# Optimization experiments

Measured on AMD Instinct MI355X. Metric: run time of the kernel, lower is better.

The kernel has to match this reference:

```python
import jax, jax.numpy as jnp
import numpy as np

N_NEURONS = 100000
N_EDGES = 5000000
N_TYPES = 64
N_DM = 512
BATCH = 16
LAYER_NUMBER = 4  # number of connectome hops


def setup_inputs() -> dict:
    key = jax.random.key(0)
    ks = jax.random.split(key, 11)
    return {
        "x": jax.random.normal(ks[0], (N_NEURONS, BATCH), dtype=jnp.float32),
        "type_weight": jax.random.normal(ks[1], (N_TYPES,), dtype=jnp.float32),
        "type_bias": jax.random.normal(ks[2], (N_TYPES,), dtype=jnp.float32),
        # shared_weights = log1p(synapse counts) -> positive; use uniform
        "edge_weights": jax.random.uniform(ks[3], (N_EDGES,), dtype=jnp.float32),
        "dm_vals": jax.random.uniform(ks[4], (N_DM,), dtype=jnp.float32),
        "fc_w": jax.random.normal(ks[5], (1, N_DM), dtype=jnp.float32) * 0.04,
        "fc_b": jax.random.normal(ks[6], (1,), dtype=jnp.float32),
        "cell_type_indices": jax.random.randint(ks[7], (N_NEURONS,), 0, N_TYPES),
        "edge_rows": jax.random.randint(ks[8], (N_EDGES,), 0, N_NEURONS),
        "edge_cols": jax.random.randint(ks[9], (N_EDGES,), 0, N_NEURONS),
        "dm_cols": jax.random.randint(ks[10], (N_DM,), 0, N_NEURONS),
    }


def reference(x, type_weight, type_bias, edge_weights, dm_vals, fc_w, fc_b,
              cell_type_indices, edge_rows, edge_cols, dm_cols):
    # RetinaConnectionLayer: per-cell-type 1->1 linear (gathered scale + bias)
    h = x * type_weight[cell_type_indices][:, None] + type_bias[cell_type_indices][:, None]
    # AdultConnectome / SparseMatrixMul: repeated sparse COO matmul h = A @ h
    # with shared per-edge weights, applied layer_number times.
    for _ in range(LAYER_NUMBER):
        contrib = edge_weights[:, None] * h[edge_cols]          # [E, B] gather
        h = jax.ops.segment_sum(contrib, edge_rows, num_segments=N_NEURONS)
    # torch.sparse.mm(decision_making_tensor, h): row-selection sparse matrix
    y = dm_vals[:, None] * h[dm_cols]                           # [N_DM, B]
    # final_fc over the decision-neuron axis
    out = y.T @ fc_w.T + fc_b                                   # [B, 1]
    return out
```

## Files before the change

### kernel.cpp

```cpp
#include <hip/hip_runtime.h>

#define NN 100000
#define NE 5000000
#define NB 16
#define NDM 512

#define RPB 1024
#define NBUCKET 98
#define CAP 55296
#define CHUNK 8192
#define NCHUNK ((NE + CHUNK - 1) / CHUNK)
#define SUB 16
#define NWAVE 16

__global__ void setup(const float* __restrict__ dmv, const int* __restrict__ dmc,
                      const float* __restrict__ fcw,
                      float* __restrict__ u0, int* __restrict__ cursor) {
    int t = threadIdx.x;
    if (t < NDM) atomicAdd(&u0[dmc[t]], dmv[t] * fcw[t]);
    if (t < NBUCKET) cursor[t] = t * CAP;
}

__global__ void scatter_fused(const int* __restrict__ er, const int* __restrict__ ec,
                              const float* __restrict__ ew,
                              const float* __restrict__ u0, float* __restrict__ u1,
                              int* __restrict__ cursor, int2* __restrict__ packed) {
    __shared__ int hist[NWAVE][NBUCKET];
    __shared__ __align__(16) int sdst[CHUNK];
    __shared__ int lbase[NBUCKET];
    __shared__ int lrank[NBUCKET];
    int tid = threadIdx.x;
    int wv = tid >> 6;
    for (int k = tid; k < NWAVE * NBUCKET; k += 1024) hist[k / NBUCKET][k % NBUCKET] = 0;
    __syncthreads();
    int base = blockIdx.x * CHUNK;
    int n = min(CHUNK, NE - base);
    const int4* ec4 = (const int4*)(ec + base);
    for (int k = tid; k < (n >> 2); k += 1024) {
        int4 c = ec4[k];
        ((int4*)sdst)[k] = c;
        atomicAdd(&hist[wv][c.x >> 10], 1);
        atomicAdd(&hist[wv][c.y >> 10], 1);
        atomicAdd(&hist[wv][c.z >> 10], 1);
        atomicAdd(&hist[wv][c.w >> 10], 1);
    }
    __syncthreads();
    for (int b = tid; b < NBUCKET; b += 1024) {
        int c = 0;
        #pragma unroll
        for (int w = 0; w < NWAVE; ++w) c += hist[w][b];
        lbase[b] = c ? atomicAdd(&cursor[b], c) : 0;
        lrank[b] = 0;
    }
    __syncthreads();
    const int4*   er4 = (const int4*)(er + base);
    const float4* ew4 = (const float4*)(ew + base);
    for (int k = tid; k < (n >> 2); k += 1024) {
        int4 r = er4[k];
        float4 w = ew4[k];
        int k4 = 4 * k;
        int d, bk, rk;
        float a;
        d = sdst[k4];     bk = d >> 10; rk = atomicAdd(&lrank[bk], 1);
        packed[lbase[bk] + rk] = make_int2(((d & 1023) << 17) | r.x, __float_as_int(w.x));
        a = u0[r.x]; if (a != 0.f) atomicAdd(&u1[d], w.x * a);
        d = sdst[k4 + 1]; bk = d >> 10; rk = atomicAdd(&lrank[bk], 1);
        packed[lbase[bk] + rk] = make_int2(((d & 1023) << 17) | r.y, __float_as_int(w.y));
        a = u0[r.y]; if (a != 0.f) atomicAdd(&u1[d], w.y * a);
        d = sdst[k4 + 2]; bk = d >> 10; rk = atomicAdd(&lrank[bk], 1);
        packed[lbase[bk] + rk] = make_int2(((d & 1023) << 17) | r.z, __float_as_int(w.z));
        a = u0[r.z]; if (a != 0.f) atomicAdd(&u1[d], w.z * a);
        d = sdst[k4 + 3]; bk = d >> 10; rk = atomicAdd(&lrank[bk], 1);
        packed[lbase[bk] + rk] = make_int2(((d & 1023) << 17) | r.w, __float_as_int(w.w));
        a = u0[r.w]; if (a != 0.f) atomicAdd(&u1[d], w.w * a);
    }
}

__global__ void spmv_sorted(const int* __restrict__ cursor,
                            const int2* __restrict__ packed,
                            const float* __restrict__ wc, float* __restrict__ wn) {
    __shared__ float acc[RPB];
    int bucket = blockIdx.x >> 4;
    int sub = blockIdx.x & (SUB - 1);
    int t = threadIdx.x;
    #pragma unroll
    for (int k = 0; k < 4; ++k) acc[t + 256 * k] = 0.f;
    __syncthreads();
    int s = bucket * CAP;
    int e = cursor[bucket];
    int cnt = e - s;
    int slice = (cnt + SUB - 1) >> 4;
    int mys = s + sub * slice;
    int mye = min(mys + slice, e);
    int i = mys + t;
    for (; i + 768 < mye; i += 1024) {
        int2 p0 = packed[i];
        int2 p1 = packed[i + 256];
        int2 p2 = packed[i + 512];
        int2 p3 = packed[i + 768];
        float v0 = __int_as_float(p0.y) * wc[p0.x & 0x1FFFF];
        float v1 = __int_as_float(p1.y) * wc[p1.x & 0x1FFFF];
        float v2 = __int_as_float(p2.y) * wc[p2.x & 0x1FFFF];
        float v3 = __int_as_float(p3.y) * wc[p3.x & 0x1FFFF];
        if (v0 != 0.f) atomicAdd(&acc[p0.x >> 17], v0);
        if (v1 != 0.f) atomicAdd(&acc[p1.x >> 17], v1);
        if (v2 != 0.f) atomicAdd(&acc[p2.x >> 17], v2);
        if (v3 != 0.f) atomicAdd(&acc[p3.x >> 17], v3);
    }
    for (; i < mye; i += 256) {
        int2 p = packed[i];
        float v = __int_as_float(p.y) * wc[p.x & 0x1FFFF];
        if (v != 0.f) atomicAdd(&acc[p.x >> 17], v);
    }
    __syncthreads();
    #pragma unroll
    for (int k = 0; k < 4; ++k) {
        int row = bucket * RPB + t + 256 * k;
        float a = acc[t + 256 * k];
        if (a != 0.f && row < NN) atomicAdd(&wn[row], a);
    }
}

__global__ void final_dot(const float* __restrict__ x, const float* __restrict__ tw,
                          const float* __restrict__ tb, const int* __restrict__ ct,
                          const float* __restrict__ u,
                          float* __restrict__ acc_out) {
    __shared__ float s[512];
    __shared__ float sred[256][4];
    __shared__ float sbias[4];
    int tid = threadIdx.x;
    int base = blockIdx.x * 512;
    int nrows = min(512, NN - base);
    float accb = 0.f;
    for (int r = tid; r < nrows; r += 256) {
        int n = base + r;
        float un = u[n];
        int t = ct[n];
        s[r] = un * tw[t];
        accb = fmaf(un, tb[t], accb);
    }
    __syncthreads();
    float a0 = 0.f, a1 = 0.f, a2 = 0.f, a3 = 0.f;
    int j = (tid & 3) * 4;
    for (int r = tid >> 2; r < nrows; r += 64) {
        float4 xv = *(const float4*)&x[(size_t)(base + r) * NB + j];
        float sv = s[r];
        a0 = fmaf(sv, xv.x, a0);
        a1 = fmaf(sv, xv.y, a1);
        a2 = fmaf(sv, xv.z, a2);
        a3 = fmaf(sv, xv.w, a3);
    }
    sred[tid][0] = a0; sred[tid][1] = a1; sred[tid][2] = a2; sred[tid][3] = a3;
    for (int off = 32; off; off >>= 1) accb += __shfl_down(accb, off);
    if ((tid & 63) == 0) sbias[tid >> 6] = accb;
    __syncthreads();
    if (tid < 16) {
        int q = tid >> 2, k = tid & 3;
        float sum = 0.f;
        for (int i = 0; i < 64; ++i) sum += sred[q + 4 * i][k];
        atomicAdd(&acc_out[tid], sum);
    }
    if (tid == 16)
        atomicAdd(&acc_out[16], sbias[0] + sbias[1] + sbias[2] + sbias[3]);
}

__global__ void finalize(const float* __restrict__ acc, const float* __restrict__ fcb,
                         float* __restrict__ out) {
    int b = threadIdx.x;
    if (b < NB) out[b] = acc[b] + acc[16] + fcb[0];
}

extern "C" void kernel_launch(void* const* d_in, const int* in_sizes, int n_in,
                              void* d_out, int out_size, void* d_ws, size_t ws_size,
                              hipStream_t stream) {
    const float* x   = (const float*)d_in[0];
    const float* tw  = (const float*)d_in[1];
    const float* tb  = (const float*)d_in[2];
    const float* ew  = (const float*)d_in[3];
    const float* dmv = (const float*)d_in[4];
    const float* fcw = (const float*)d_in[5];
    const float* fcb = (const float*)d_in[6];
    const int* ct  = (const int*)d_in[7];
    const int* er  = (const int*)d_in[8];
    const int* ec  = (const int*)d_in[9];
    const int* dmc = (const int*)d_in[10];
    float* out = (float*)d_out;

    char* ws = (char*)d_ws;
    float* u   = (float*)ws;
    float* acc = u + 5 * (size_t)NN;
    size_t zero_bytes = (5 * (size_t)NN + 32) * 4;
    ws += zero_bytes;
    int* cursor = (int*)ws;         ws += 128 * 4;
    ws = (char*)(((uintptr_t)ws + 15) & ~(uintptr_t)15);
    int2* packed = (int2*)ws;

    hipMemsetAsync(u, 0, zero_bytes, stream);

    setup<<<1, 512, 0, stream>>>(dmv, dmc, fcw, u, cursor);

    scatter_fused<<<NCHUNK, 1024, 0, stream>>>(er, ec, ew, u, u + NN, cursor, packed);

    for (int l = 1; l < 4; ++l) {
        spmv_sorted<<<NBUCKET * SUB, 256, 0, stream>>>(cursor, packed,
                                                       u + (size_t)l * NN,
                                                       u + (size_t)(l + 1) * NN);
    }

    final_dot<<<(NN + 511) / 512, 256, 0, stream>>>(x, tw, tb, ct, u + 4 * (size_t)NN, acc);
    finalize<<<1, 64, 0, stream>>>(acc, fcb, out);
}
```

Measured before the change: 170.5 us.

## Stage bucket-sorted edges in shared memory before coalesced global write-out

The scatter kernel now does the edge and weight loads in a single pass, holding the edges in registers, and takes each edge's local rank from the histogram atomic. A shared-memory prefix sum then places every entry into a block-local sorted buffer, which is copied to the global packed array in bucket-contiguous runs. This replaces the global scatter that used a per-edge LDS rank atomic and issued random 8-byte stores. In exchange the kernel uses more shared memory (about 64KB plus extra), needs more registers, and adds several barriers for the scan.

```diff
diff --git a/kernel.cpp b/kernel.cpp
--- a/kernel.cpp
+++ b/kernel.cpp
@@ -21,58 +21,100 @@
     if (t < NBUCKET) cursor[t] = t * CAP;
 }
 
-__global__ void scatter_fused(const int* __restrict__ er, const int* __restrict__ ec,
-                              const float* __restrict__ ew,
-                              const float* __restrict__ u0, float* __restrict__ u1,
-                              int* __restrict__ cursor, int2* __restrict__ packed) {
+__global__ void __launch_bounds__(1024, 8)
+scatter_fused(const int* __restrict__ er, const int* __restrict__ ec,
+              const float* __restrict__ ew,
+              const float* __restrict__ u0, float* __restrict__ u1,
+              int* __restrict__ cursor, int2* __restrict__ packed) {
     __shared__ int hist[NWAVE][NBUCKET];
-    __shared__ __align__(16) int sdst[CHUNK];
-    __shared__ int lbase[NBUCKET];
-    __shared__ int lrank[NBUCKET];
+    __shared__ int2 pval[CHUNK];
+    __shared__ unsigned char sbk[CHUNK];
+    __shared__ int lbloc[128];
+    __shared__ int gbase[NBUCKET];
+    __shared__ int ctot[NBUCKET];
     int tid = threadIdx.x;
     int wv = tid >> 6;
     for (int k = tid; k < NWAVE * NBUCKET; k += 1024) hist[k / NBUCKET][k % NBUCKET] = 0;
     __syncthreads();
     int base = blockIdx.x * CHUNK;
     int n = min(CHUNK, NE - base);
-    const int4* ec4 = (const int4*)(ec + base);
-    for (int k = tid; k < (n >> 2); k += 1024) {
-        int4 c = ec4[k];
-        ((int4*)sdst)[k] = c;
-        atomicAdd(&hist[wv][c.x >> 10], 1);
-        atomicAdd(&hist[wv][c.y >> 10], 1);
-        atomicAdd(&hist[wv][c.z >> 10], 1);
-        atomicAdd(&hist[wv][c.w >> 10], 1);
-    }
-    __syncthreads();
-    for (int b = tid; b < NBUCKET; b += 1024) {
+    int nq = n >> 2;
+    const int4*   ec4 = (const int4*)(ec + base);
+    const int4*   er4 = (const int4*)(er + base);
+    const float4* ew4 = (const float4*)(ew + base);
+
+    int2 ent[2][4];
+    int  meta[2][4];
+    #pragma unroll
+    for (int g = 0; g < 2; ++g) {
+        int k = tid + g * 1024;
+        if (k < nq) {
+            int4 c = ec4[k];
+            int4 r = er4[k];
+            float4 w = ew4[k];
+            int cc[4] = {c.x, c.y, c.z, c.w};
+            int rr[4] = {r.x, r.y, r.z, r.w};
+            float ww[4] = {w.x, w.y, w.z, w.w};
+            #pragma unroll
+            for (int j = 0; j < 4; ++j) {
+                int d = cc[j];
+                int bk = d >> 10;
+                int lp = atomicAdd(&hist[wv][bk], 1);
+                ent[g][j] = make_int2(((d & 1023) << 17) | rr[j], __float_as_int(ww[j]));
+                meta[g][j] = (lp << 7) | bk;
+                float a = u0[rr[j]];
+                if (a != 0.f) atomicAdd(&u1[d], ww[j] * a);
+            }
+        }
+    }
+    __syncthreads();
+    if (tid < NBUCKET) {
         int c = 0;
         #pragma unroll
-        for (int w = 0; w < NWAVE; ++w) c += hist[w][b];
-        lbase[b] = c ? atomicAdd(&cursor[b], c) : 0;
-        lrank[b] = 0;
-    }
-    __syncthreads();
-    const int4*   er4 = (const int4*)(er + base);
-    const float4* ew4 = (const float4*)(ew + base);
-    for (int k = tid; k < (n >> 2); k += 1024) {
-        int4 r = er4[k];
-        float4 w = ew4[k];
-        int k4 = 4 * k;
-        int d, bk, rk;
-        float a;
-        d = sdst[k4];     bk = d >> 10; rk = atomicAdd(&lrank[bk], 1);
-        packed[lbase[bk] + rk] = make_int2(((d & 1023) << 17) | r.x, __float_as_int(w.x));
-        a = u0[r.x]; if (a != 0.f) atomicAdd(&u1[d], w.x * a);
-        d = sdst[k4 + 1]; bk = d >> 10; rk = atomicAdd(&lrank[bk], 1);
-        packed[lbase[bk] + rk] = make_int2(((d & 1023) << 17) | r.y, __float_as_int(w.y));
-        a = u0[r.y]; if (a != 0.f) atomicAdd(&u1[d], w.y * a);
-        d = sdst[k4 + 2]; bk = d >> 10; rk = atomicAdd(&lrank[bk], 1);
-        packed[lbase[bk] + rk] = make_int2(((d & 1023) << 17) | r.z, __float_as_int(w.z));
-        a = u0[r.z]; if (a != 0.f) atomicAdd(&u1[d], w.z * a);
-        d = sdst[k4 + 3]; bk = d >> 10; rk = atomicAdd(&lrank[bk], 1);
-        packed[lbase[bk] + rk] = make_int2(((d & 1023) << 17) | r.w, __float_as_int(w.w));
-        a = u0[r.w]; if (a != 0.f) atomicAdd(&u1[d], w.w * a);
+        for (int w = 0; w < NWAVE; ++w) c += hist[w][tid];
+        ctot[tid] = c;
+        gbase[tid] = c ? atomicAdd(&cursor[tid], c) : 0;
+    }
+    __syncthreads();
+    if (tid < 128) lbloc[tid] = (tid < NBUCKET) ? ctot[tid] : 0;
+    __syncthreads();
+    for (int off = 1; off < 128; off <<= 1) {
+        int v = 0;
+        if (tid < 128 && tid >= off) v = lbloc[tid - off];
+        __syncthreads();
+        if (tid < 128) lbloc[tid] += v;
+        __syncthreads();
+    }
+    if (tid < NBUCKET) {
+        int lb = lbloc[tid] - ctot[tid];
+        lbloc[tid] = lb;
+        int c = lb;
+        #pragma unroll
+        for (int w = 0; w < NWAVE; ++w) {
+            int t = hist[w][tid];
+            hist[w][tid] = c;
+            c += t;
+        }
+    }
+    __syncthreads();
+    #pragma unroll
+    for (int g = 0; g < 2; ++g) {
+        int k = tid + g * 1024;
+        if (k < nq) {
+            #pragma unroll
+            for (int j = 0; j < 4; ++j) {
+                int m = meta[g][j];
+                int bk = m & 127;
+                int pos = hist[wv][bk] + (m >> 7);
+                pval[pos] = ent[g][j];
+                sbk[pos] = (unsigned char)bk;
+            }
+        }
+    }
+    __syncthreads();
+    for (int i = tid; i < n; i += 1024) {
+        int bk = sbk[i];
+        packed[gbase[bk] + (i - lbloc[bk])] = pval[i];
     }
 }
 
```

Result: faster. 155.5 us (-8.8%).
